# Performance work log

Measured on AMD Instinct MI355X. Metric: run time of the kernel, lower is better.

Reference implementation:

```python
import jax, jax.numpy as jnp
import numpy as np

B, N, D, H = 4, 1024, 1024, 16
Dh = D // H


def setup_inputs() -> dict:
    key = jax.random.key(0)
    ks = jax.random.split(key, 5)
    w = 0.02
    return {
        "x": jax.random.normal(ks[0], (B, N, D), dtype=jnp.float32),
        "Wq": jax.random.normal(ks[1], (D, D), dtype=jnp.float32) * w,
        "bq": jnp.zeros((D,), dtype=jnp.float32),
        "Wk": jax.random.normal(ks[2], (D, D), dtype=jnp.float32) * w,
        "bk": jnp.zeros((D,), dtype=jnp.float32),
        "Wv": jax.random.normal(ks[3], (D, D), dtype=jnp.float32) * w,
        "bv": jnp.zeros((D,), dtype=jnp.float32),
        "Wc": jax.random.normal(ks[4], (D, D), dtype=jnp.float32) * w,
        "bc": jnp.zeros((D,), dtype=jnp.float32),
    }


def reference(x, Wq, bq, Wk, bk, Wv, bv, Wc, bc):
    # q/k/v projections: nn.Linear computes x @ W.T + b
    q = jnp.einsum("bnd,ed->bne", x, Wq) + bq
    k = jnp.einsum("bnd,ed->bne", x, Wk) + bk
    v = jnp.einsum("bnd,ed->bne", x, Wv) + bv
    # split heads: [B,N,D] -> [B,H,N,Dh]
    qh = q.reshape(B, N, H, Dh).transpose(0, 2, 1, 3)
    kh = k.reshape(B, N, H, Dh).transpose(0, 2, 1, 3)
    vh = v.reshape(B, N, H, Dh).transpose(0, 2, 1, 3)
    # NOTE (faithful quirk): original uses scale = q.size(1) = seq_len N,
    # not head_dim, so scores are scaled by N**-0.5.
    scale = jnp.float32(N) ** -0.5
    scores = jnp.einsum("bhnd,bhmd->bhnm", qh, kh) * scale  # [B,H,N,N]
    attn = jax.nn.softmax(scores, axis=-1)
    # attn_dropout = 0.0 -> identity
    o = jnp.einsum("bhnm,bhmd->bhnd", attn, vh)  # [B,H,N,Dh]
    # NOTE (faithful quirk): original does v.resize(original_size) on the
    # contiguous [B,H,N,Dh] tensor, reinterpreting memory as [B,N,D]
    # WITHOUT permuting heads back. Replicate exactly:
    o = o.reshape(B, N, D)
    out = jnp.einsum("bnd,ed->bne", o, Wc) + bc
    return out
```

## Files before the change

kernel.cpp:

```cpp
#include <hip/hip_runtime.h>
#include <cstddef>
#include <cstdint>

#define B_  4
#define N_  1024
#define D_  1024
#define H_  16
#define DH  64
#define M_  4096

typedef __attribute__((ext_vector_type(4))) float   f32x4;
typedef __attribute__((ext_vector_type(8))) __bf16  bf16x8;
typedef __attribute__((ext_vector_type(4))) __bf16  bf16x4;

#define MFMA(a, b, c) __builtin_amdgcn_mfma_f32_16x16x32_bf16((a), (b), (c), 0, 0, 0)
#define GLDS(gp, lp) __builtin_amdgcn_global_load_lds( \
    (__attribute__((address_space(1))) void*)(gp),     \
    (__attribute__((address_space(3))) void*)(lp), 16, 0, 0)

__global__ __launch_bounds__(256) void convert_k(
    const float* __restrict__ x,  const float* __restrict__ Wq,
    const float* __restrict__ Wk, const float* __restrict__ Wv,
    const float* __restrict__ Wc,
    __bf16* __restrict__ xb, __bf16* __restrict__ wqkvb,
    __bf16* __restrict__ wcb)
{
    const unsigned u = blockIdx.x * 256u + threadIdx.x;
    const unsigned e = u * 8u;
    const float* src;
    __bf16* dst;
    if (e < 4194304u) { src = x + e; dst = xb + e; }
    else {
        const unsigned t2 = e - 4194304u;
        const unsigned wsel = t2 >> 20;
        const unsigned wo = t2 & 1048575u;
        src = (wsel == 0 ? Wq : wsel == 1 ? Wk : wsel == 2 ? Wv : Wc) + wo;
        dst = (wsel < 3 ? wqkvb + (size_t)wsel * 1048576u : wcb) + wo;
    }
    const float4 f0 = *(const float4*)(src);
    const float4 f1 = *(const float4*)(src + 4);
    bf16x8 r;
    r[0] = (__bf16)f0.x; r[1] = (__bf16)f0.y; r[2] = (__bf16)f0.z; r[3] = (__bf16)f0.w;
    r[4] = (__bf16)f1.x; r[5] = (__bf16)f1.y; r[6] = (__bf16)f1.z; r[7] = (__bf16)f1.w;
    *(bf16x8*)dst = r;
}

template <typename OutT, bool HEADS>
__global__ __launch_bounds__(256, 3) void gemm_nt(
    const __bf16* __restrict__ A, const __bf16* __restrict__ Wb,
    const float* __restrict__ b0, const float* __restrict__ b1,
    const float* __restrict__ b2, OutT* __restrict__ Cb,
    int Nc, int K)
{
    __shared__ __bf16 As[4096];
    __shared__ __bf16 Bs[4096];

    const int tid  = threadIdx.x;
    const int w    = tid >> 6;
    const int lane = tid & 63;
    const int quad = lane >> 4;
    const int l15  = lane & 15;
    const int wr   = w >> 1, wc = w & 1;

    const int m0 = blockIdx.y * 128;
    const int n0 = blockIdx.x * 128;
    const int z  = blockIdx.z;

    const __bf16* W    = Wb + (size_t)z * Nc * K;
    const float*  bias = (z == 0) ? b0 : (z == 1) ? b1 : b2;
    OutT*         C    = Cb + (size_t)z * M_ * Nc;

    const int c1 = w * 128 + lane, c2 = c1 + 64;
    const size_t aoff1 = (size_t)(m0 + ((c1 >> 6) * 16) + (c1 & 15)) * K + (((c1 >> 4) & 3) * 8);
    const size_t aoff2 = (size_t)(m0 + ((c2 >> 6) * 16) + (c2 & 15)) * K + (((c2 >> 4) & 3) * 8);
    const size_t boff1 = (size_t)(n0 + ((c1 >> 6) * 16) + (c1 & 15)) * K + (((c1 >> 4) & 3) * 8);
    const size_t boff2 = (size_t)(n0 + ((c2 >> 6) * 16) + (c2 & 15)) * K + (((c2 >> 4) & 3) * 8);
    __bf16* asdst1 = As + w * 1024;
    __bf16* asdst2 = As + w * 1024 + 512;
    __bf16* bsdst1 = Bs + w * 1024;
    __bf16* bsdst2 = Bs + w * 1024 + 512;

    f32x4 acc[4][4];
    #pragma unroll
    for (int i = 0; i < 4; ++i)
        #pragma unroll
        for (int j = 0; j < 4; ++j)
            acc[i][j] = (f32x4){0.f, 0.f, 0.f, 0.f};

    for (int k0 = 0; k0 < K; k0 += 32) {
        GLDS(A + aoff1 + k0, asdst1);
        GLDS(A + aoff2 + k0, asdst2);
        GLDS(W + boff1 + k0, bsdst1);
        GLDS(W + boff2 + k0, bsdst2);
        __syncthreads();

        bf16x8 af[4], bf[4];
        #pragma unroll
        for (int t = 0; t < 4; ++t) {
            af[t] = *(const bf16x8*)(As + ((wr * 4 + t) * 64 + quad * 16 + l15) * 8);
            bf[t] = *(const bf16x8*)(Bs + ((wc * 4 + t) * 64 + quad * 16 + l15) * 8);
        }
        #pragma unroll
        for (int mt = 0; mt < 4; ++mt)
            #pragma unroll
            for (int nt = 0; nt < 4; ++nt)
                acc[mt][nt] = MFMA(af[mt], bf[nt], acc[mt][nt]);
        __syncthreads();
    }

    float bv[4];
    #pragma unroll
    for (int nt = 0; nt < 4; ++nt)
        bv[nt] = bias[n0 + wc * 64 + nt * 16 + l15];
    #pragma unroll
    for (int mt = 0; mt < 4; ++mt) {
        #pragma unroll
        for (int r = 0; r < 4; ++r) {
            const int row = m0 + wr * 64 + mt * 16 + quad * 4 + r;
            #pragma unroll
            for (int nt = 0; nt < 4; ++nt) {
                const int col = n0 + wc * 64 + nt * 16 + l15;
                const float val = acc[mt][nt][r] + bv[nt];
                if (HEADS) {
                    const size_t idx = (((size_t)(row >> 10) * H_ + (col >> 6)) * N_
                                        + (row & 1023)) * DH + (col & 63);
                    C[idx] = (OutT)val;
                } else {
                    C[(size_t)row * Nc + col] = (OutT)val;
                }
            }
        }
    }
}

__global__ __launch_bounds__(256) void transpose_v(
    const __bf16* __restrict__ v, __bf16* __restrict__ vT)
{
    __shared__ __bf16 Ts[64][72];
    const int tid = threadIdx.x;
    const int b  = blockIdx.x >> 8;
    const int h  = (blockIdx.x >> 4) & 15;
    const int nt = blockIdx.x & 15;
    const int r  = tid >> 2;
    const int c0 = (tid & 3) * 16;

    const __bf16* src = v + ((size_t)(b * H_ + h) * N_ + nt * 64 + r) * DH + c0;
    *(bf16x8*)&Ts[r][c0]     = *(const bf16x8*)(src);
    *(bf16x8*)&Ts[r][c0 + 8] = *(const bf16x8*)(src + 8);
    __syncthreads();

    const int dh = tid >> 2;
    __bf16* dst = vT + ((size_t)(b * H_ + h) * DH + dh) * N_ + nt * 64 + c0;
    bf16x8 o0, o1;
    #pragma unroll
    for (int j = 0; j < 8; ++j) o0[j] = Ts[c0 + j][dh];
    #pragma unroll
    for (int j = 0; j < 8; ++j) o1[j] = Ts[c0 + 8 + j][dh];
    *(bf16x8*)dst       = o0;
    *(bf16x8*)(dst + 8) = o1;
}

#define SP  68
#define SC2 0.04508422f

__global__ __launch_bounds__(256, 4) void attn_mfma(
    const __bf16* __restrict__ qh, const __bf16* __restrict__ kh,
    const __bf16* __restrict__ vT, __bf16* __restrict__ ob)
{
    __shared__ __bf16 Ks[4096];
    __shared__ __bf16 Vs[4096];
    __shared__ float  Ps[4][16 * SP];

    const int tid  = threadIdx.x;
    const int w    = tid >> 6;
    const int lane = tid & 63;
    const int quad = lane >> 4;
    const int l15  = lane & 15;

    const int bh = blockIdx.x & 63;
    const int qt = blockIdx.x >> 6;
    const int b  = bh >> 4;
    const int h  = bh & 15;

    const __bf16* qp = qh + ((size_t)(b * H_ + h) * N_ + qt * 64 + w * 16 + l15) * DH + quad * 8;
    const bf16x8 qf0 = *(const bf16x8*)(qp);
    const bf16x8 qf1 = *(const bf16x8*)(qp + 32);

    const int c1 = tid, c2 = tid + 256;
    const int nt1 = c1 >> 7, ko1 = (c1 >> 4) & 7, l1 = c1 & 15;
    const int nt2 = c2 >> 7, ko2 = (c2 >> 4) & 7, l2 = c2 & 15;
    const __bf16* khead = kh + (size_t)(b * H_ + h) * N_ * DH;
    const __bf16* vhead = vT + (size_t)(b * H_ + h) * DH * N_;
    const size_t koff1 = (size_t)(nt1 * 16 + l1) * DH + ko1 * 8;
    const size_t koff2 = (size_t)(nt2 * 16 + l2) * DH + ko2 * 8;
    const size_t voff1 = (size_t)(nt1 * 16 + l1) * N_ + ko1 * 8;
    const size_t voff2 = (size_t)(nt2 * 16 + l2) * N_ + ko2 * 8;
    __bf16* ksdst1 = Ks + w * 512;
    __bf16* ksdst2 = Ks + 2048 + w * 512;
    __bf16* vsdst1 = Vs + w * 512;
    __bf16* vsdst2 = Vs + 2048 + w * 512;

    float psum[4] = {0.f, 0.f, 0.f, 0.f};
    f32x4 Ov[4];
    #pragma unroll
    for (int nt = 0; nt < 4; ++nt) Ov[nt] = (f32x4){0.f, 0.f, 0.f, 0.f};

    for (int kt = 0; kt < 16; ++kt) {
        GLDS(khead + (size_t)kt * 64 * DH + koff1, ksdst1);
        GLDS(khead + (size_t)kt * 64 * DH + koff2, ksdst2);
        GLDS(vhead + (size_t)kt * 64 + voff1, vsdst1);
        GLDS(vhead + (size_t)kt * 64 + voff2, vsdst2);
        __syncthreads();

        f32x4 sa[4];
        #pragma unroll
        for (int nt = 0; nt < 4; ++nt) {
            const bf16x8 kf0 = *(const bf16x8*)(Ks + (nt * 128 + quad * 16 + l15) * 8);
            const bf16x8 kf1 = *(const bf16x8*)(Ks + (nt * 128 + (quad + 4) * 16 + l15) * 8);
            sa[nt] = (f32x4){0.f, 0.f, 0.f, 0.f};
            sa[nt] = MFMA(qf0, kf0, sa[nt]);
            sa[nt] = MFMA(qf1, kf1, sa[nt]);
        }

        #pragma unroll
        for (int nt = 0; nt < 4; ++nt) {
            #pragma unroll
            for (int r = 0; r < 4; ++r) {
                const float p = __builtin_exp2f(sa[nt][r] * SC2);
                psum[r] += p;
                Ps[w][(quad * 4 + r) * SP + nt * 16 + l15] = p;
            }
        }

        #pragma unroll
        for (int kw = 0; kw < 2; ++kw) {
            const f32x4 pa = *(const f32x4*)&Ps[w][l15 * SP + kw * 32 + quad * 8];
            const f32x4 pb = *(const f32x4*)&Ps[w][l15 * SP + kw * 32 + quad * 8 + 4];
            bf16x8 pf;
            #pragma unroll
            for (int j = 0; j < 4; ++j) { pf[j] = (__bf16)pa[j]; pf[4 + j] = (__bf16)pb[j]; }
            #pragma unroll
            for (int nt = 0; nt < 4; ++nt) {
                const bf16x8 vf = *(const bf16x8*)(Vs + (nt * 128 + (kw * 4 + quad) * 16 + l15) * 8);
                Ov[nt] = MFMA(pf, vf, Ov[nt]);
            }
        }
        __syncthreads();
    }

    float lrow[4];
    #pragma unroll
    for (int r = 0; r < 4; ++r) {
        float lt = psum[r];
        lt += __shfl_xor(lt, 1);
        lt += __shfl_xor(lt, 2);
        lt += __shfl_xor(lt, 4);
        lt += __shfl_xor(lt, 8);
        lrow[r] = lt;
    }

    #pragma unroll
    for (int r = 0; r < 4; ++r) {
        const float inv = 1.0f / lrow[r];
        const int row = qt * 64 + w * 16 + quad * 4 + r;
        __bf16* op = ob + ((size_t)(b * H_ + h) * N_ + row) * DH + l15;
        #pragma unroll
        for (int nt = 0; nt < 4; ++nt)
            op[nt * 16] = (__bf16)(Ov[nt][r] * inv);
    }
}

extern "C" void kernel_launch(void* const* d_in, const int* in_sizes, int n_in,
                              void* d_out, int out_size, void* d_ws, size_t ws_size,
                              hipStream_t stream) {
    const float* x  = (const float*)d_in[0];
    const float* Wq = (const float*)d_in[1];
    const float* bq = (const float*)d_in[2];
    const float* Wk = (const float*)d_in[3];
    const float* bk = (const float*)d_in[4];
    const float* Wv = (const float*)d_in[5];
    const float* bv = (const float*)d_in[6];
    const float* Wc = (const float*)d_in[7];
    const float* bc = (const float*)d_in[8];
    float* out = (float*)d_out;

    char* base = (char*)d_ws;
    __bf16* xb    = (__bf16*)(base);
    __bf16* wqkvb = (__bf16*)(base + (size_t)8  * 1048576);
    __bf16* wcb   = (__bf16*)(base + (size_t)14 * 1048576);
    __bf16* qkvb  = (__bf16*)(base + (size_t)16 * 1048576);
    __bf16* vTb   = (__bf16*)(base + (size_t)40 * 1048576);
    __bf16* obf   = (__bf16*)(base);

    __bf16* qhb = qkvb;
    __bf16* khb = qkvb + (size_t)M_ * D_;
    __bf16* vhb = qkvb + (size_t)2 * M_ * D_;

    convert_k<<<dim3(4096), dim3(256), 0, stream>>>(
        x, Wq, Wk, Wv, Wc, xb, wqkvb, wcb);

    gemm_nt<__bf16, true><<<dim3(8, 32, 3), dim3(256), 0, stream>>>(
        xb, wqkvb, bq, bk, bv, qkvb, D_, D_);

    transpose_v<<<dim3(1024), dim3(256), 0, stream>>>(vhb, vTb);

    attn_mfma<<<dim3(1024), dim3(256), 0, stream>>>(qhb, khb, vTb, obf);

    gemm_nt<float, false><<<dim3(8, 32, 1), dim3(256), 0, stream>>>(
        obf, wcb, bc, bc, bc, out, D_, D_);
}
```

Before: 218.2 us.

## Fuse V transpose into QKV GEMM and shrink GEMM tiles to 64x128

Replaces the 128x128 GEMM with a 64x128 tile variant that allows higher occupancy (launch bound 6) and launches twice as many blocks. For the V projection, it computes W_v·x^T directly so the output lands already transposed in the vT layout, which removes the separate transpose kernel and its extra pass over memory. Smaller tiles lower data reuse per block, and the transposed V store writes along N in 16-element runs per row, which may coalesce less well.

```diff
diff --git a/kernel.cpp b/kernel.cpp
--- a/kernel.cpp
+++ b/kernel.cpp
@@ -45,14 +45,14 @@
     *(bf16x8*)dst = r;
 }
 
-template <typename OutT, bool HEADS>
-__global__ __launch_bounds__(256, 3) void gemm_nt(
-    const __bf16* __restrict__ A, const __bf16* __restrict__ Wb,
+template <int MODE, typename OutT>
+__global__ __launch_bounds__(256, 6) void gemm64(
+    const __bf16* __restrict__ A0, const __bf16* __restrict__ Wb,
     const float* __restrict__ b0, const float* __restrict__ b1,
     const float* __restrict__ b2, OutT* __restrict__ Cb,
-    int Nc, int K)
+    OutT* __restrict__ vTp, int K)
 {
-    __shared__ __bf16 As[4096];
+    __shared__ __bf16 As[2048];
     __shared__ __bf16 Bs[4096];
 
     const int tid  = threadIdx.x;
@@ -62,102 +62,100 @@
     const int l15  = lane & 15;
     const int wr   = w >> 1, wc = w & 1;
 
-    const int m0 = blockIdx.y * 128;
-    const int n0 = blockIdx.x * 128;
-    const int z  = blockIdx.z;
-
-    const __bf16* W    = Wb + (size_t)z * Nc * K;
-    const float*  bias = (z == 0) ? b0 : (z == 1) ? b1 : b2;
-    OutT*         C    = Cb + (size_t)z * M_ * Nc;
-
-    const int c1 = w * 128 + lane, c2 = c1 + 64;
-    const size_t aoff1 = (size_t)(m0 + ((c1 >> 6) * 16) + (c1 & 15)) * K + (((c1 >> 4) & 3) * 8);
-    const size_t aoff2 = (size_t)(m0 + ((c2 >> 6) * 16) + (c2 & 15)) * K + (((c2 >> 4) & 3) * 8);
-    const size_t boff1 = (size_t)(n0 + ((c1 >> 6) * 16) + (c1 & 15)) * K + (((c1 >> 4) & 3) * 8);
-    const size_t boff2 = (size_t)(n0 + ((c2 >> 6) * 16) + (c2 & 15)) * K + (((c2 >> 4) & 3) * 8);
-    __bf16* asdst1 = As + w * 1024;
-    __bf16* asdst2 = As + w * 1024 + 512;
-    __bf16* bsdst1 = Bs + w * 1024;
-    __bf16* bsdst2 = Bs + w * 1024 + 512;
-
-    f32x4 acc[4][4];
+    const int z  = (MODE == 1) ? blockIdx.z : 0;
+    const bool VT = (MODE == 1) && (z == 2);
+
+    int m0, n0;
+    if (VT) { m0 = (blockIdx.y & 15) * 64; n0 = (((blockIdx.y >> 4) * 8) + blockIdx.x) * 128; }
+    else    { m0 = blockIdx.y * 64;        n0 = blockIdx.x * 128; }
+
+    const __bf16* Aptr;
+    const __bf16* Bptr;
+    if (MODE == 1) {
+        if (VT) { Aptr = Wb + (size_t)2 * D_ * D_; Bptr = A0; }
+        else    { Aptr = A0; Bptr = Wb + (size_t)z * D_ * D_; }
+    } else { Aptr = A0; Bptr = Wb; }
+
+    const int Tt = tid >> 6, ko = (tid >> 4) & 3, l = tid & 15;
+    const size_t aoff  = (size_t)(m0 + Tt * 16 + l) * K + ko * 8;
+    const size_t boff1 = (size_t)(n0 + Tt * 16 + l) * K + ko * 8;
+    const size_t boff2 = boff1 + (size_t)64 * K;
+    __bf16* adst  = As + w * 512;
+    __bf16* bdst1 = Bs + w * 512;
+    __bf16* bdst2 = Bs + 2048 + w * 512;
+
+    f32x4 acc[2][4];
     #pragma unroll
-    for (int i = 0; i < 4; ++i)
+    for (int i = 0; i < 2; ++i)
         #pragma unroll
         for (int j = 0; j < 4; ++j)
             acc[i][j] = (f32x4){0.f, 0.f, 0.f, 0.f};
 
     for (int k0 = 0; k0 < K; k0 += 32) {
-        GLDS(A + aoff1 + k0, asdst1);
-        GLDS(A + aoff2 + k0, asdst2);
-        GLDS(W + boff1 + k0, bsdst1);
-        GLDS(W + boff2 + k0, bsdst2);
+        GLDS(Aptr + aoff  + k0, adst);
+        GLDS(Bptr + boff1 + k0, bdst1);
+        GLDS(Bptr + boff2 + k0, bdst2);
         __syncthreads();
 
-        bf16x8 af[4], bf[4];
-        #pragma unroll
-        for (int t = 0; t < 4; ++t) {
-            af[t] = *(const bf16x8*)(As + ((wr * 4 + t) * 64 + quad * 16 + l15) * 8);
-            bf[t] = *(const bf16x8*)(Bs + ((wc * 4 + t) * 64 + quad * 16 + l15) * 8);
-        }
-        #pragma unroll
-        for (int mt = 0; mt < 4; ++mt)
+        bf16x8 af[2], bf[4];
+        #pragma unroll
+        for (int mt = 0; mt < 2; ++mt)
+            af[mt] = *(const bf16x8*)(As + (((wr * 2 + mt) * 4 + quad) * 16 + l15) * 8);
+        #pragma unroll
+        for (int nt = 0; nt < 4; ++nt)
+            bf[nt] = *(const bf16x8*)(Bs + (((wc * 4 + nt) * 4 + quad) * 16 + l15) * 8);
+        #pragma unroll
+        for (int mt = 0; mt < 2; ++mt)
             #pragma unroll
             for (int nt = 0; nt < 4; ++nt)
                 acc[mt][nt] = MFMA(af[mt], bf[nt], acc[mt][nt]);
         __syncthreads();
     }
 
-    float bv[4];
-    #pragma unroll
-    for (int nt = 0; nt < 4; ++nt)
-        bv[nt] = bias[n0 + wc * 64 + nt * 16 + l15];
-    #pragma unroll
-    for (int mt = 0; mt < 4; ++mt) {
-        #pragma unroll
-        for (int r = 0; r < 4; ++r) {
-            const int row = m0 + wr * 64 + mt * 16 + quad * 4 + r;
-            #pragma unroll
-            for (int nt = 0; nt < 4; ++nt) {
-                const int col = n0 + wc * 64 + nt * 16 + l15;
-                const float val = acc[mt][nt][r] + bv[nt];
-                if (HEADS) {
-                    const size_t idx = (((size_t)(row >> 10) * H_ + (col >> 6)) * N_
-                                        + (row & 1023)) * DH + (col & 63);
-                    C[idx] = (OutT)val;
-                } else {
-                    C[(size_t)row * Nc + col] = (OutT)val;
+    if (!VT) {
+        const float* bias = (MODE == 0) ? b0 : (z == 0 ? b0 : b1);
+        float bvv[4];
+        #pragma unroll
+        for (int nt = 0; nt < 4; ++nt)
+            bvv[nt] = bias[n0 + wc * 64 + nt * 16 + l15];
+        #pragma unroll
+        for (int mt = 0; mt < 2; ++mt) {
+            #pragma unroll
+            for (int r = 0; r < 4; ++r) {
+                const int row = m0 + (wr * 2 + mt) * 16 + quad * 4 + r;
+                #pragma unroll
+                for (int nt = 0; nt < 4; ++nt) {
+                    const int col = n0 + wc * 64 + nt * 16 + l15;
+                    const float val = acc[mt][nt][r] + bvv[nt];
+                    if (MODE == 1) {
+                        OutT* C = Cb + (size_t)z * M_ * D_;
+                        const size_t idx = (((size_t)(row >> 10) * H_ + (col >> 6)) * N_
+                                            + (row & 1023)) * DH + (col & 63);
+                        C[idx] = (OutT)val;
+                    } else {
+                        Cb[(size_t)row * D_ + col] = (OutT)val;
+                    }
                 }
             }
         }
-    }
-}
-
-__global__ __launch_bounds__(256) void transpose_v(
-    const __bf16* __restrict__ v, __bf16* __restrict__ vT)
-{
-    __shared__ __bf16 Ts[64][72];
-    const int tid = threadIdx.x;
-    const int b  = blockIdx.x >> 8;
-    const int h  = (blockIdx.x >> 4) & 15;
-    const int nt = blockIdx.x & 15;
-    const int r  = tid >> 2;
-    const int c0 = (tid & 3) * 16;
-
-    const __bf16* src = v + ((size_t)(b * H_ + h) * N_ + nt * 64 + r) * DH + c0;
-    *(bf16x8*)&Ts[r][c0]     = *(const bf16x8*)(src);
-    *(bf16x8*)&Ts[r][c0 + 8] = *(const bf16x8*)(src + 8);
-    __syncthreads();
-
-    const int dh = tid >> 2;
-    __bf16* dst = vT + ((size_t)(b * H_ + h) * DH + dh) * N_ + nt * 64 + c0;
-    bf16x8 o0, o1;
-    #pragma unroll
-    for (int j = 0; j < 8; ++j) o0[j] = Ts[c0 + j][dh];
-    #pragma unroll
-    for (int j = 0; j < 8; ++j) o1[j] = Ts[c0 + 8 + j][dh];
-    *(bf16x8*)dst       = o0;
-    *(bf16x8*)(dst + 8) = o1;
+    } else {
+        #pragma unroll
+        for (int mt = 0; mt < 2; ++mt) {
+            #pragma unroll
+            for (int r = 0; r < 4; ++r) {
+                const int row = m0 + (wr * 2 + mt) * 16 + quad * 4 + r;
+                const float brow = b2[row];
+                #pragma unroll
+                for (int nt = 0; nt < 4; ++nt) {
+                    const int col = n0 + wc * 64 + nt * 16 + l15;
+                    const float val = acc[mt][nt][r] + brow;
+                    const size_t idx = (((size_t)(col >> 10) * H_ + (row >> 6)) * DH
+                                        + (row & 63)) * N_ + (col & 1023);
+                    vTp[idx] = (OutT)val;
+                }
+            }
+        }
+    }
 }
 
 #define SP  68
@@ -294,18 +292,15 @@
 
     __bf16* qhb = qkvb;
     __bf16* khb = qkvb + (size_t)M_ * D_;
-    __bf16* vhb = qkvb + (size_t)2 * M_ * D_;
 
     convert_k<<<dim3(4096), dim3(256), 0, stream>>>(
         x, Wq, Wk, Wv, Wc, xb, wqkvb, wcb);
 
-    gemm_nt<__bf16, true><<<dim3(8, 32, 3), dim3(256), 0, stream>>>(
-        xb, wqkvb, bq, bk, bv, qkvb, D_, D_);
-
-    transpose_v<<<dim3(1024), dim3(256), 0, stream>>>(vhb, vTb);
+    gemm64<1, __bf16><<<dim3(8, 64, 3), dim3(256), 0, stream>>>(
+        xb, wqkvb, bq, bk, bv, qkvb, vTb, D_);
 
     attn_mfma<<<dim3(1024), dim3(256), 0, stream>>>(qhb, khb, vTb, obf);
 
-    gemm_nt<float, false><<<dim3(8, 32, 1), dim3(256), 0, stream>>>(
-        obf, wcb, bc, bc, bc, out, D_, D_);
+    gemm64<0, float><<<dim3(8, 64, 1), dim3(256), 0, stream>>>(
+        obf, wcb, bc, bc, bc, out, out, D_);
 }
```

Measured after the change: 229.1 us. 1.05x slower.
